# Performance work log

Measured on AMD Instinct MI355X. Metric: run time of the kernel, lower is better.

Reference implementation:

```python
import jax, jax.numpy as jnp
import numpy as np

P = 512       # input_shape
HD = 256      # hidden_dim
N = 65536     # number of samples
LAM1 = 1.0
LAM3 = 1.0


def setup_inputs() -> dict:
    key = jax.random.key(0)
    ks = jax.random.split(key, 12)
    def lin(kw, kb, out_d, in_d):
        lim = 1.0 / np.sqrt(in_d)
        W = jax.random.uniform(kw, (out_d, in_d), jnp.float32, -lim, lim)
        b = jax.random.uniform(kb, (out_d,), jnp.float32, -lim, lim)
        return W, b
    W1, b1 = lin(ks[0], ks[1], 200, P + HD)
    W12, b12 = lin(ks[2], ks[3], 100, 200)
    W13, b13 = lin(ks[4], ks[5], 100, 100)
    W2, b2 = lin(ks[6], ks[7], P, 100)
    return {
        "input": jax.random.normal(ks[8], (N, P), jnp.float32),
        "h": jax.random.normal(ks[9], (N, HD), jnp.float32),
        "W1": W1, "b1": b1, "W12": W12, "b12": b12,
        "W13": W13, "b13": b13, "W2": W2, "b2": b2,
        "idx0": 0, "idx1": N,
    }


def reference(input, h, W1, b1, W12, b12, W13, b13, W2, b2, idx0, idx1):
    n = input.shape[0]
    hs = h[idx0:idx1]                                   # [N, HD]
    x = jnp.concatenate([input, hs], axis=1)            # [N, P+HD]
    x = jax.nn.relu(x @ W1.T + b1)                      # dropout = identity (eval)
    x = jax.nn.relu(x @ W12.T + b12)
    x = jax.nn.relu(x @ W13.T + b13)
    f_x_h = x @ W2.T + b2                               # [N, P]
    mu = jnp.mean(hs, axis=0)                           # [HD]
    # S = mean_i <h_i, h_i> : vectorized sum-of-squares (replaces Python loop)
    S = jnp.mean(jnp.sum(hs * hs, axis=1))
    part0 = jnp.linalg.norm(f_x_h[:-1] - input[1:]) / (n - 1)
    part1 = LAM1 * jnp.sum(jnp.abs(mu)) / HD
    part2 = LAM1 * jnp.abs(S / HD - 1.0)
    part3 = LAM3 * jnp.mean(jnp.sum(jnp.abs(hs[1:] - hs[:-1]), axis=1)) / HD
    return (f_x_h, part0, part1, part2, part3)
```

## Files before the change

kernel.cpp:

```cpp
#include <hip/hip_runtime.h>

typedef __bf16 bf16;
typedef __bf16 bf16x4 __attribute__((ext_vector_type(4)));
typedef __bf16 bf16x8 __attribute__((ext_vector_type(8)));
typedef float f32x4 __attribute__((ext_vector_type(4)));

#define N_ROWS 65536

#define W1_E   159744
#define W12_E  25088
#define W13_E  14336
#define W2_E   65536
#define WP_TOTAL (W1_E + W12_E + W13_E + W2_E)
#define W12_OFF_B 319488
#define W13_OFF_B 369664
#define W2_OFF_B  398336
#define BP_OFF_BYTES (WP_TOTAL * 2)
#define BP_FLOATS 944
#define ACC_OFF_BYTES (BP_OFF_BYTES + BP_FLOATS * 4)
#define NCOPY 16
#define P0_IDX (NCOPY * 256)
#define S_IDX0 (P0_IDX + 1)
#define P3_IDX0 (S_IDX0 + NCOPY)
#define ACC_FLOATS (P3_IDX0 + NCOPY)

__device__ inline int swz4(int r) { return (r ^ (r >> 2)) & 3; }

__global__ void pack_kernel(const float* __restrict__ W1, const float* __restrict__ b1,
                            const float* __restrict__ W12, const float* __restrict__ b12,
                            const float* __restrict__ W13, const float* __restrict__ b13,
                            const float* __restrict__ W2, const float* __restrict__ b2,
                            bf16* __restrict__ wp, float* __restrict__ bp) {
  int i = blockIdx.x * 256 + threadIdx.x;
  if (i < WP_TOTAL) {
    float v = 0.0f;
    if (i < W1_E) {
      int s = i / 6656, b = i - s * 6656;
      int r = b >> 5, w = b & 31;
      int k = s * 32 + (((w >> 3) ^ swz4(r)) << 3) + (w & 7);
      if (r < 200) v = W1[r * 768 + k];
    } else if (i < W1_E + W12_E) {
      int j = i - W1_E;
      int s = j / 3584, b = j - s * 3584;
      int r = b >> 5, w = b & 31;
      int k = s * 32 + (((w >> 3) ^ swz4(r)) << 3) + (w & 7);
      if (r < 100 && k < 200) v = W12[r * 200 + k];
    } else if (i < W1_E + W12_E + W13_E) {
      int j = i - (W1_E + W12_E);
      int s = j / 3584, b = j - s * 3584;
      int r = b >> 5, w = b & 31;
      int k = s * 32 + (((w >> 3) ^ swz4(r)) << 3) + (w & 7);
      if (r < 100 && k < 100) v = W13[r * 100 + k];
    } else {
      int j = i - (W1_E + W12_E + W13_E);
      int g = j >> 14, rest = j & 16383;
      int s = rest >> 12, b = rest & 4095;
      int r = b >> 5, w = b & 31;
      int o = g * 128 + r;
      int k = s * 32 + (((w >> 3) ^ swz4(r)) << 3) + (w & 7);
      if (k < 100) v = W2[o * 100 + k];
    }
    wp[i] = (bf16)v;
  } else {
    int j = i - WP_TOTAL;
    if (j < BP_FLOATS) {
      float v = 0.0f;
      if (j < 208)      { if (j < 200) v = b1[j]; }
      else if (j < 320) { int o = j - 208; if (o < 100) v = b12[o]; }
      else if (j < 432) { int o = j - 320; if (o < 100) v = b13[o]; }
      else              { v = b2[j - 432]; }
      bp[j] = v;
    }
  }
}

#define MFMA(a, b, c) __builtin_amdgcn_mfma_f32_16x16x32_bf16((a), (b), (c), 0, 0, 0)

template<int BYTES>
__device__ inline void stage(const char* __restrict__ src, bf16* __restrict__ dstw, int tid) {
  char* dst = (char*)dstw;
  const int off0 = (tid >> 6) * 1024 + (tid & 63) * 16;
  constexpr int NCH = (BYTES + 4095) / 4096;
#pragma unroll
  for (int j = 0; j < NCH; j++) {
    const int off = j * 4096 + off0;
    if ((BYTES & 4095) == 0 || off < BYTES)
      __builtin_amdgcn_global_load_lds(
          (const __attribute__((address_space(1))) void*)(src + off),
          (__attribute__((address_space(3))) void*)(dst + off),
          16, 0, 0);
  }
}

__global__ __launch_bounds__(256, 2) void mlp_main(
    const float* __restrict__ input, const float* __restrict__ h,
    const bf16* __restrict__ wp, const float* __restrict__ bp,
    float* __restrict__ out, float* __restrict__ p0_accum) {
  __shared__ __align__(16) bf16 acts[4][3712];
  __shared__ __align__(16) bf16 wbuf[2][6656];
  __shared__ __align__(16) bf16 abuf[4][2048];
  __shared__ float p0red[4];

  const int tid = threadIdx.x;
  const int lane = tid & 63;
  const int wave = tid >> 6;
  const int c16 = lane & 15;
  const int quad = lane >> 4;
  const int m0 = blockIdx.x * 64 + wave * 16;
  const int qs8 = (quad ^ swz4(c16)) * 8;

  const char* wpb = (const char*)wp;
  const float* b1p  = bp;
  const float* b12p = bp + 208;
  const float* b13p = bp + 320;
  const float* b2p  = bp + 432;

  bf16* actw = &acts[wave][0];
  bf16* aw = &abuf[wave][0];

  f32x4 acc1[13];
#pragma unroll
  for (int t = 0; t < 13; t++) acc1[t] = (f32x4){0.f, 0.f, 0.f, 0.f};

  f32x4 ar[8];
  auto loadA = [&](int kb) {
#pragma unroll
    for (int i = 0; i < 8; i++) {
      const int row = 2 * i + (lane >> 5);
      const int col = (lane & 31) * 4;
      const float* src = (kb < 4)
          ? (input + (size_t)(m0 + row) * 512 + kb * 128 + col)
          : (h + (size_t)(m0 + row) * 256 + (kb - 4) * 128 + col);
      ar[i] = *(const f32x4*)src;
    }
  };
  auto writeA = [&]() {
    const int kk = (lane & 31) >> 3;
    const int q  = ((lane & 31) >> 1) & 3;
    const int sub = (lane & 1) * 4;
#pragma unroll
    for (int i = 0; i < 8; i++) {
      const int row = 2 * i + (lane >> 5);
      bf16x4 cv;
#pragma unroll
      for (int c = 0; c < 4; c++) cv[c] = (bf16)ar[i][c];
      *(bf16x4*)(aw + kk * 512 + row * 32 + ((q ^ swz4(row)) * 8) + sub) = cv;
    }
  };

  stage<13312>(wpb, wbuf[0], tid);
  loadA(0);

  for (int kb = 0; kb < 6; kb++) {
    writeA();
    __syncthreads();
#pragma unroll
    for (int j = 0; j < 4; j++) {
      const int ks = kb * 4 + j;
      if (j == 0 && kb + 1 < 6) loadA(kb + 1);
      if (ks + 1 < 24) stage<13312>(wpb + (ks + 1) * 13312, wbuf[(ks + 1) & 1], tid);
      bf16x8 a = *(const bf16x8*)(aw + j * 512 + c16 * 32 + qs8);
      const bf16* buf = wbuf[ks & 1];
#pragma unroll
      for (int t = 0; t < 13; t++) {
        bf16x8 bb = *(const bf16x8*)(buf + (t * 16 + c16) * 32 + qs8);
        acc1[t] = MFMA(a, bb, acc1[t]);
      }
      __syncthreads();
    }
  }
#pragma unroll
  for (int t = 0; t < 13; t++) {
    const float bias = b1p[t * 16 + c16];
#pragma unroll
    for (int r = 0; r < 4; r++)
      actw[(quad * 4 + r) * 232 + t * 16 + c16] = (bf16)fmaxf(acc1[t][r] + bias, 0.0f);
  }
  for (int idx = lane; idx < 256; idx += 64)
    actw[(idx >> 4) * 232 + 208 + (idx & 15)] = (bf16)0.0f;

  f32x4 acc2[7];
#pragma unroll
  for (int t = 0; t < 7; t++) acc2[t] = (f32x4){0.f, 0.f, 0.f, 0.f};

  stage<7168>(wpb + W12_OFF_B, wbuf[0], tid);
  __syncthreads();
#pragma unroll
  for (int ks = 0; ks < 7; ks++) {
    if (ks + 1 < 7) stage<7168>(wpb + W12_OFF_B + (ks + 1) * 7168, wbuf[(ks + 1) & 1], tid);
    bf16x8 a = *(const bf16x8*)(actw + c16 * 232 + ks * 32 + quad * 8);
    const bf16* buf = wbuf[ks & 1];
#pragma unroll
    for (int t = 0; t < 7; t++) {
      bf16x8 bb = *(const bf16x8*)(buf + (t * 16 + c16) * 32 + qs8);
      acc2[t] = MFMA(a, bb, acc2[t]);
    }
    __syncthreads();
  }
#pragma unroll
  for (int t = 0; t < 7; t++) {
    const float bias = b12p[t * 16 + c16];
#pragma unroll
    for (int r = 0; r < 4; r++)
      actw[(quad * 4 + r) * 136 + t * 16 + c16] = (bf16)fmaxf(acc2[t][r] + bias, 0.0f);
  }
  for (int idx = lane; idx < 256; idx += 64)
    actw[(idx >> 4) * 136 + 112 + (idx & 15)] = (bf16)0.0f;

  f32x4 acc3[7];
#pragma unroll
  for (int t = 0; t < 7; t++) acc3[t] = (f32x4){0.f, 0.f, 0.f, 0.f};

  stage<7168>(wpb + W13_OFF_B, wbuf[0], tid);
  __syncthreads();
#pragma unroll
  for (int ks = 0; ks < 4; ks++) {
    if (ks + 1 < 4) stage<7168>(wpb + W13_OFF_B + (ks + 1) * 7168, wbuf[(ks + 1) & 1], tid);
    bf16x8 a = *(const bf16x8*)(actw + c16 * 136 + ks * 32 + quad * 8);
    const bf16* buf = wbuf[ks & 1];
#pragma unroll
    for (int t = 0; t < 7; t++) {
      bf16x8 bb = *(const bf16x8*)(buf + (t * 16 + c16) * 32 + qs8);
      acc3[t] = MFMA(a, bb, acc3[t]);
    }
    __syncthreads();
  }
#pragma unroll
  for (int t = 0; t < 7; t++) {
    const float bias = b13p[t * 16 + c16];
#pragma unroll
    for (int r = 0; r < 4; r++)
      actw[(quad * 4 + r) * 136 + t * 16 + c16] = (bf16)fmaxf(acc3[t][r] + bias, 0.0f);
  }
  for (int idx = lane; idx < 256; idx += 64)
    actw[(idx >> 4) * 136 + 112 + (idx & 15)] = (bf16)0.0f;

  float p0local = 0.0f;
  for (int g = 0; g < 4; g++) {
    f32x4 acc4[8];
#pragma unroll
    for (int t = 0; t < 8; t++) acc4[t] = (f32x4){0.f, 0.f, 0.f, 0.f};

    const char* Wg = wpb + W2_OFF_B + g * 32768;
    stage<8192>(Wg, wbuf[0], tid);
    __syncthreads();
#pragma unroll
    for (int ks = 0; ks < 4; ks++) {
      if (ks + 1 < 4) stage<8192>(Wg + (ks + 1) * 8192, wbuf[(ks + 1) & 1], tid);
      bf16x8 a = *(const bf16x8*)(actw + c16 * 136 + ks * 32 + quad * 8);
      const bf16* buf = wbuf[ks & 1];
#pragma unroll
      for (int t = 0; t < 8; t++) {
        bf16x8 bb = *(const bf16x8*)(buf + (t * 16 + c16) * 32 + qs8);
        acc4[t] = MFMA(a, bb, acc4[t]);
      }
      __syncthreads();
    }
#pragma unroll
    for (int t = 0; t < 8; t++) {
      const int o = g * 128 + t * 16 + c16;
      const float bias = b2p[o];
#pragma unroll
      for (int r = 0; r < 4; r++) {
        const int grow = m0 + quad * 4 + r;
        float v = acc4[t][r] + bias;
        out[(size_t)grow * 512 + o] = v;
        if (grow < N_ROWS - 1) {
          float d = v - input[(size_t)(grow + 1) * 512 + o];
          p0local += d * d;
        }
      }
    }
  }
#pragma unroll
  for (int off = 32; off > 0; off >>= 1) p0local += __shfl_down(p0local, off);
  if (lane == 0) p0red[wave] = p0local;
  __syncthreads();
  if (tid == 0) atomicAdd(p0_accum, p0red[0] + p0red[1] + p0red[2] + p0red[3]);
}

__global__ __launch_bounds__(256) void reduce_h(const float* __restrict__ h, float* __restrict__ acc) {
  __shared__ f32x4 cbuf[256];
  __shared__ float redS[256];
  __shared__ float redP[256];
  const int t = threadIdx.x;
  const int c = t & 63;
  const int rg = t >> 6;
  const int start = blockIdx.x * 32 + rg * 8;

  const float* base = h + (size_t)start * 256 + c * 4;
  f32x4 v[9];
#pragma unroll
  for (int r = 0; r < 8; r++) v[r] = *(const f32x4*)(base + (size_t)r * 256);
  if (start + 8 < N_ROWS) v[8] = *(const f32x4*)(base + (size_t)8 * 256);
  else                    v[8] = v[7];

  f32x4 csum = (f32x4){0.f, 0.f, 0.f, 0.f};
  f32x4 s2v  = (f32x4){0.f, 0.f, 0.f, 0.f};
  f32x4 p3v  = (f32x4){0.f, 0.f, 0.f, 0.f};
#pragma unroll
  for (int r = 0; r < 8; r++) {
    csum += v[r];
    s2v  += v[r] * v[r];
    f32x4 d = v[r + 1] - v[r];
#pragma unroll
    for (int i = 0; i < 4; i++) p3v[i] += __builtin_fabsf(d[i]);
  }
  cbuf[t] = csum;
  redS[t] = s2v[0] + s2v[1] + s2v[2] + s2v[3];
  redP[t] = p3v[0] + p3v[1] + p3v[2] + p3v[3];
  __syncthreads();
  if (rg == 0) {
    f32x4 s = cbuf[c] + cbuf[c + 64] + cbuf[c + 128] + cbuf[c + 192];
    float* dst = acc + (blockIdx.x & (NCOPY - 1)) * 256 + 4 * c;
    atomicAdd(dst + 0, s[0]);
    atomicAdd(dst + 1, s[1]);
    atomicAdd(dst + 2, s[2]);
    atomicAdd(dst + 3, s[3]);
  }
  for (int st = 128; st > 0; st >>= 1) {
    if (t < st) { redS[t] += redS[t + st]; redP[t] += redP[t + st]; }
    __syncthreads();
  }
  if (t == 0) {
    atomicAdd(&acc[S_IDX0 + (blockIdx.x & (NCOPY - 1))], redS[0]);
    atomicAdd(&acc[P3_IDX0 + (blockIdx.x & (NCOPY - 1))], redP[0]);
  }
}

__global__ void finalize(const float* __restrict__ acc, float* __restrict__ out) {
  __shared__ float red[256];
  const int t = threadIdx.x;
  float s = 0.0f;
#pragma unroll
  for (int j = 0; j < NCOPY; j++) s += acc[j * 256 + t];
  red[t] = fabsf(s);
  __syncthreads();
  for (int st = 128; st > 0; st >>= 1) {
    if (t < st) red[t] += red[t + st];
    __syncthreads();
  }
  if (t == 0) {
    float Ssum = 0.f, Psum = 0.f;
#pragma unroll
    for (int j = 0; j < NCOPY; j++) { Ssum += acc[S_IDX0 + j]; Psum += acc[P3_IDX0 + j]; }
    out[(size_t)N_ROWS * 512 + 0] = sqrtf(acc[P0_IDX]) / 65535.0f;
    out[(size_t)N_ROWS * 512 + 1] = red[0] / 65536.0f / 256.0f;
    out[(size_t)N_ROWS * 512 + 2] = fabsf(Ssum / (65536.0f * 256.0f) - 1.0f);
    out[(size_t)N_ROWS * 512 + 3] = Psum / (65535.0f * 256.0f);
  }
}

extern "C" void kernel_launch(void* const* d_in, const int* in_sizes, int n_in,
                              void* d_out, int out_size, void* d_ws, size_t ws_size,
                              hipStream_t stream) {
  const float* input = (const float*)d_in[0];
  const float* h   = (const float*)d_in[1];
  const float* W1  = (const float*)d_in[2];
  const float* b1  = (const float*)d_in[3];
  const float* W12 = (const float*)d_in[4];
  const float* b12 = (const float*)d_in[5];
  const float* W13 = (const float*)d_in[6];
  const float* b13 = (const float*)d_in[7];
  const float* W2  = (const float*)d_in[8];
  const float* b2  = (const float*)d_in[9];
  float* out = (float*)d_out;

  bf16* wp = (bf16*)d_ws;
  float* bp = (float*)((char*)d_ws + BP_OFF_BYTES);
  float* acc = (float*)((char*)d_ws + ACC_OFF_BYTES);

  hipMemsetAsync(acc, 0, ACC_FLOATS * sizeof(float), stream);
  pack_kernel<<<(WP_TOTAL + BP_FLOATS + 255) / 256, 256, 0, stream>>>(
      W1, b1, W12, b12, W13, b13, W2, b2, wp, bp);
  mlp_main<<<N_ROWS / 64, 256, 0, stream>>>(input, h, wp, bp, out, acc + P0_IDX);
  reduce_h<<<N_ROWS / 32, 256, 0, stream>>>(h, acc);
  finalize<<<1, 256, 0, stream>>>(acc, out);
}
```

Measured before the change: 431.8 us.

## Fuse h statistics reduction into MLP kernel and alias A staging buffer

```diff
diff --git a/kernel.cpp b/kernel.cpp
--- a/kernel.cpp
+++ b/kernel.cpp
@@ -95,11 +95,10 @@
 __global__ __launch_bounds__(256, 2) void mlp_main(
     const float* __restrict__ input, const float* __restrict__ h,
     const bf16* __restrict__ wp, const float* __restrict__ bp,
-    float* __restrict__ out, float* __restrict__ p0_accum) {
+    float* __restrict__ out, float* __restrict__ acc) {
   __shared__ __align__(16) bf16 acts[4][3712];
   __shared__ __align__(16) bf16 wbuf[2][6656];
-  __shared__ __align__(16) bf16 abuf[4][2048];
-  __shared__ float p0red[4];
+  __shared__ float wred[4][3];
 
   const int tid = threadIdx.x;
   const int lane = tid & 63;
@@ -116,7 +115,11 @@
   const float* b2p  = bp + 432;
 
   bf16* actw = &acts[wave][0];
-  bf16* aw = &abuf[wave][0];
+  bf16* aw = actw;
+
+  f32x4 csA = (f32x4){0.f, 0.f, 0.f, 0.f};
+  f32x4 csB = (f32x4){0.f, 0.f, 0.f, 0.f};
+  float s2loc = 0.0f, p3loc = 0.0f;
 
   f32x4 acc1[13];
 #pragma unroll
@@ -153,6 +156,25 @@
 
   for (int kb = 0; kb < 6; kb++) {
     writeA();
+    if (kb >= 4) {
+      f32x4* cs = (kb == 4) ? &csA : &csB;
+#pragma unroll
+      for (int i = 0; i < 8; i++) {
+        f32x4 oth;
+#pragma unroll
+        for (int c = 0; c < 4; c++) oth[c] = __shfl_xor(ar[i][c], 32);
+        *cs += ar[i];
+#pragma unroll
+        for (int c = 0; c < 4; c++) s2loc += ar[i][c] * ar[i][c];
+        if (lane < 32) {
+#pragma unroll
+          for (int c = 0; c < 4; c++) p3loc += __builtin_fabsf(oth[c] - ar[i][c]);
+        } else if (i >= 1) {
+#pragma unroll
+          for (int c = 0; c < 4; c++) p3loc += __builtin_fabsf(oth[c] - ar[i - 1][c]);
+        }
+      }
+    }
     __syncthreads();
 #pragma unroll
     for (int j = 0; j < 4; j++) {
@@ -272,59 +294,45 @@
       }
     }
   }
-#pragma unroll
-  for (int off = 32; off > 0; off >>= 1) p0local += __shfl_down(p0local, off);
-  if (lane == 0) p0red[wave] = p0local;
+
+  {
+    const int p = tid >> 6, cq = tid & 63;
+    const int rowA = blockIdx.x * 64 + p * 16 + 15;
+    if (rowA + 1 < N_ROWS) {
+      f32x4 a = *(const f32x4*)(h + (size_t)rowA * 256 + cq * 4);
+      f32x4 b = *(const f32x4*)(h + (size_t)(rowA + 1) * 256 + cq * 4);
+#pragma unroll
+      for (int c = 0; c < 4; c++) p3loc += __builtin_fabsf(b[c] - a[c]);
+    }
+  }
+#pragma unroll
+  for (int c = 0; c < 4; c++) {
+    csA[c] += __shfl_xor(csA[c], 32);
+    csB[c] += __shfl_xor(csB[c], 32);
+  }
+  f32x4* hred = (f32x4*)&acts[0][0];
+  if (lane < 32) hred[wave * 64 + lane] = csA;
+  else           hred[wave * 64 + 32 + (lane & 31)] = csB;
+#pragma unroll
+  for (int off = 32; off > 0; off >>= 1) {
+    p0local += __shfl_down(p0local, off);
+    s2loc   += __shfl_down(s2loc, off);
+    p3loc   += __shfl_down(p3loc, off);
+  }
+  if (lane == 0) { wred[wave][0] = p0local; wred[wave][1] = s2loc; wred[wave][2] = p3loc; }
   __syncthreads();
-  if (tid == 0) atomicAdd(p0_accum, p0red[0] + p0red[1] + p0red[2] + p0red[3]);
-}
-
-__global__ __launch_bounds__(256) void reduce_h(const float* __restrict__ h, float* __restrict__ acc) {
-  __shared__ f32x4 cbuf[256];
-  __shared__ float redS[256];
-  __shared__ float redP[256];
-  const int t = threadIdx.x;
-  const int c = t & 63;
-  const int rg = t >> 6;
-  const int start = blockIdx.x * 32 + rg * 8;
-
-  const float* base = h + (size_t)start * 256 + c * 4;
-  f32x4 v[9];
-#pragma unroll
-  for (int r = 0; r < 8; r++) v[r] = *(const f32x4*)(base + (size_t)r * 256);
-  if (start + 8 < N_ROWS) v[8] = *(const f32x4*)(base + (size_t)8 * 256);
-  else                    v[8] = v[7];
-
-  f32x4 csum = (f32x4){0.f, 0.f, 0.f, 0.f};
-  f32x4 s2v  = (f32x4){0.f, 0.f, 0.f, 0.f};
-  f32x4 p3v  = (f32x4){0.f, 0.f, 0.f, 0.f};
-#pragma unroll
-  for (int r = 0; r < 8; r++) {
-    csum += v[r];
-    s2v  += v[r] * v[r];
-    f32x4 d = v[r + 1] - v[r];
-#pragma unroll
-    for (int i = 0; i < 4; i++) p3v[i] += __builtin_fabsf(d[i]);
-  }
-  cbuf[t] = csum;
-  redS[t] = s2v[0] + s2v[1] + s2v[2] + s2v[3];
-  redP[t] = p3v[0] + p3v[1] + p3v[2] + p3v[3];
-  __syncthreads();
-  if (rg == 0) {
-    f32x4 s = cbuf[c] + cbuf[c + 64] + cbuf[c + 128] + cbuf[c + 192];
-    float* dst = acc + (blockIdx.x & (NCOPY - 1)) * 256 + 4 * c;
-    atomicAdd(dst + 0, s[0]);
-    atomicAdd(dst + 1, s[1]);
-    atomicAdd(dst + 2, s[2]);
-    atomicAdd(dst + 3, s[3]);
-  }
-  for (int st = 128; st > 0; st >>= 1) {
-    if (t < st) { redS[t] += redS[t + st]; redP[t] += redP[t + st]; }
-    __syncthreads();
-  }
-  if (t == 0) {
-    atomicAdd(&acc[S_IDX0 + (blockIdx.x & (NCOPY - 1))], redS[0]);
-    atomicAdd(&acc[P3_IDX0 + (blockIdx.x & (NCOPY - 1))], redP[0]);
+  if (tid < 64) {
+    f32x4 tot = hred[tid] + hred[64 + tid] + hred[128 + tid] + hred[192 + tid];
+    float* dst = acc + (blockIdx.x & (NCOPY - 1)) * 256 + tid * 4;
+    atomicAdd(dst + 0, tot[0]);
+    atomicAdd(dst + 1, tot[1]);
+    atomicAdd(dst + 2, tot[2]);
+    atomicAdd(dst + 3, tot[3]);
+  }
+  if (tid == 0) {
+    atomicAdd(&acc[P0_IDX], wred[0][0] + wred[1][0] + wred[2][0] + wred[3][0]);
+    atomicAdd(&acc[S_IDX0 + (blockIdx.x & (NCOPY - 1))], wred[0][1] + wred[1][1] + wred[2][1] + wred[3][1]);
+    atomicAdd(&acc[P3_IDX0 + (blockIdx.x & (NCOPY - 1))], wred[0][2] + wred[1][2] + wred[2][2] + wred[3][2]);
   }
 }
 
@@ -373,7 +381,6 @@
   hipMemsetAsync(acc, 0, ACC_FLOATS * sizeof(float), stream);
   pack_kernel<<<(WP_TOTAL + BP_FLOATS + 255) / 256, 256, 0, stream>>>(
       W1, b1, W12, b12, W13, b13, W2, b2, wp, bp);
-  mlp_main<<<N_ROWS / 64, 256, 0, stream>>>(input, h, wp, bp, out, acc + P0_IDX);
-  reduce_h<<<N_ROWS / 32, 256, 0, stream>>>(h, acc);
+  mlp_main<<<N_ROWS / 64, 256, 0, stream>>>(input, h, wp, bp, out, acc);
   finalize<<<1, 256, 0, stream>>>(acc, out);
 }
```

After: 408.5 us. -5.4%, faster.
